# Optimization experiments

Measured on AMD Instinct MI355X. Metric: run time of the kernel, lower is better.

## Reference

```python
import jax, jax.numpy as jnp
import numpy as np
from jax import lax

B, S, T = 256, 128, 64
IN, MID, HID = 4, 128, 512
NH = 4  # attention heads


def setup_inputs() -> dict:
    key = jax.random.key(0)
    ks = iter(jax.random.split(key, 64))
    def p(*shape):
        return jax.random.normal(next(ks), shape, jnp.float32) * 0.05
    d = {}
    d["src"] = jax.random.normal(next(ks), (B, S, IN), jnp.float32)
    d["trg"] = jax.random.normal(next(ks), (B, T, IN), jnp.float32)
    # fc_in: IN -> MID//4 -> MID//2 -> MID
    d["fi_w1"] = p(MID // 4, IN); d["fi_b1"] = p(MID // 4)
    d["fi_w2"] = p(MID // 2, MID // 4); d["fi_b2"] = p(MID // 2)
    d["fi_w3"] = p(MID, MID // 2); d["fi_b3"] = p(MID)
    # encoder: 2-layer bidirectional LSTM (layer0 in=MID, layer1 in=2*HID)
    for name, ind in [("e0", MID), ("e1", 2 * HID)]:
        for sfx in ["f", "b"]:
            d[name + sfx + "_wih"] = p(4 * HID, ind)
            d[name + sfx + "_whh"] = p(4 * HID, HID)
            d[name + sfx + "_bih"] = p(4 * HID)
            d[name + sfx + "_bhh"] = p(4 * HID)
    d["attnfc_w"] = p(MID, 2 * HID); d["attnfc_b"] = p(MID)
    d["inproj_w"] = p(3 * MID, MID); d["inproj_b"] = p(3 * MID)
    d["outproj_w"] = p(MID, MID); d["outproj_b"] = p(MID)
    # decoder: 2-layer unidirectional LSTM (layer0 in=MID, layer1 in=HID)
    for name, ind in [("d0", MID), ("d1", HID)]:
        d[name + "_wih"] = p(4 * HID, ind)
        d[name + "_whh"] = p(4 * HID, HID)
        d[name + "_bih"] = p(4 * HID)
        d[name + "_bhh"] = p(4 * HID)
    # fc_out: HID -> MID//2 -> MID//4 -> IN
    d["fo_w1"] = p(MID // 2, HID); d["fo_b1"] = p(MID // 2)
    d["fo_w2"] = p(MID // 4, MID // 2); d["fo_b2"] = p(MID // 4)
    d["fo_w3"] = p(IN, MID // 4); d["fo_b3"] = p(IN)
    return d


def _gelu(x):
    return jax.nn.gelu(x, approximate=False)  # torch default GELU is exact


def _mlp3(x, w1, b1, w2, b2, w3, b3):
    h = _gelu(x @ w1.T + b1)
    h = _gelu(h @ w2.T + b2)
    return h @ w3.T + b3


def _lstm(x, h0, c0, wih, whh, bih, bhh, reverse=False):
    """PyTorch-semantics LSTM layer. x: (B,T,in) -> (hs (B,T,H), h_T, c_T)."""
    xg = jnp.einsum('bti,gi->btg', x, wih) + (bih + bhh)  # fold input GEMM over time
    def step(carry, xt):
        h, c = carry
        g = xt + h @ whh.T
        i, f, gg, o = jnp.split(g, 4, axis=-1)  # torch gate order: i,f,g,o
        c = jax.nn.sigmoid(f) * c + jax.nn.sigmoid(i) * jnp.tanh(gg)
        h = jax.nn.sigmoid(o) * jnp.tanh(c)
        return (h, c), h
    (h, c), hs = lax.scan(step, (h0, c0), jnp.swapaxes(xg, 0, 1), reverse=reverse)
    return jnp.swapaxes(hs, 0, 1), h, c


def _mha(q_in, kv, inproj_w, inproj_b, outproj_w, outproj_b):
    E = q_in.shape[-1]
    dh = E // NH
    wq, wk, wv = jnp.split(inproj_w, 3, axis=0)
    bq, bk, bv = jnp.split(inproj_b, 3)
    q = q_in @ wq.T + bq
    k = kv @ wk.T + bk
    v = kv @ wv.T + bv
    hd = lambda x: x.reshape(x.shape[0], x.shape[1], NH, dh)
    scores = jnp.einsum('bqhd,bkhd->bhqk', hd(q), hd(k)) * (1.0 / float(np.sqrt(dh)))
    a = jax.nn.softmax(scores, axis=-1)
    o = jnp.einsum('bhqk,bkhd->bqhd', a, hd(v)).reshape(q.shape)
    return o @ outproj_w.T + outproj_b


def reference(src, trg,
              fi_w1, fi_b1, fi_w2, fi_b2, fi_w3, fi_b3,
              e0f_wih, e0f_whh, e0f_bih, e0f_bhh, e0b_wih, e0b_whh, e0b_bih, e0b_bhh,
              e1f_wih, e1f_whh, e1f_bih, e1f_bhh, e1b_wih, e1b_whh, e1b_bih, e1b_bhh,
              attnfc_w, attnfc_b, inproj_w, inproj_b, outproj_w, outproj_b,
              d0_wih, d0_whh, d0_bih, d0_bhh, d1_wih, d1_whh, d1_bih, d1_bhh,
              fo_w1, fo_b1, fo_w2, fo_b2, fo_w3, fo_b3):
    bsz = src.shape[0]
    z = jnp.zeros((bsz, HID), src.dtype)
    enc_embed = _mlp3(src, fi_w1, fi_b1, fi_w2, fi_b2, fi_w3, fi_b3)
    # encoder layer 0 (bidirectional)
    l0f, hf0, cf0 = _lstm(enc_embed, z, z, e0f_wih, e0f_whh, e0f_bih, e0f_bhh)
    l0b, hb0, cb0 = _lstm(enc_embed, z, z, e0b_wih, e0b_whh, e0b_bih, e0b_bhh, reverse=True)
    x1 = jnp.concatenate([l0f, l0b], axis=-1)
    # encoder layer 1 (bidirectional)
    l1f, hf1, cf1 = _lstm(x1, z, z, e1f_wih, e1f_whh, e1f_bih, e1f_bhh)
    l1b, hb1, cb1 = _lstm(x1, z, z, e1b_wih, e1b_whh, e1b_bih, e1b_bhh, reverse=True)
    enc_out = jnp.concatenate([l1f, l1b], axis=-1)  # (B,S,2H)
    # h.view(L,2,B,H).sum(dim=1): sum forward+backward final states per layer
    h_l0, c_l0 = hf0 + hb0, cf0 + cb0
    h_l1, c_l1 = hf1 + hb1, cf1 + cb1
    proj_enc = jnp.tanh(enc_out @ attnfc_w.T + attnfc_b)  # (B,S,MID)
    # teacher_forcing_ratio = 1.0 -> decoder inputs are exactly trg[:, 0:T]
    inp = _mlp3(trg, fi_w1, fi_b1, fi_w2, fi_b2, fi_w3, fi_b3)  # (B,T,MID)
    attn_out = _mha(inp, proj_enc, inproj_w, inproj_b, outproj_w, outproj_b)
    dec_input = inp + attn_out
    d0, _, _ = _lstm(dec_input, h_l0, c_l0, d0_wih, d0_whh, d0_bih, d0_bhh)
    d1, _, _ = _lstm(d0, h_l1, c_l1, d1_wih, d1_whh, d1_bih, d1_bhh)
    delta = _mlp3(d1, fo_w1, fo_b1, fo_w2, fo_b2, fo_w3, fo_b3)
    return trg + delta  # pred_t = trg[:, t-1] + delta_t
```

## Files before the change

### kernel.cpp

```cpp
#include <hip/hip_runtime.h>
#include <cstdint>
#include <cstddef>
#include <cstdio>

typedef __bf16 bf16;
typedef __bf16 bf16x8 __attribute__((ext_vector_type(8)));
typedef __bf16 bf16x4 __attribute__((ext_vector_type(4)));
typedef float f32x4 __attribute__((ext_vector_type(4)));

#define DEVFN __device__ __forceinline__

DEVFN float geluf(float x) { return 0.5f * x * (1.0f + erff(x * 0.70710678118654752f)); }
DEVFN float sigmoidf(float x) { return 1.0f / (1.0f + expf(-x)); }

template <int WGM, int WGN, int ACT, bool RES>
__launch_bounds__(WGM * WGN * 64)
__global__ void gemm_bt(const bf16* __restrict__ A, const bf16* __restrict__ W,
                        const float* __restrict__ bias, const bf16* __restrict__ Rsd,
                        bf16* __restrict__ C, int M, int N, int K) {
  constexpr int BM = WGM * 64, BN = WGN * 64, T = WGM * WGN * 64;
  constexpr int NA = BM * 4 / T, NB = BN * 4 / T;
  __shared__ __align__(16) char ldsA[BM * 64];
  __shared__ __align__(16) char ldsB[BN * 64];
  const int tid = threadIdx.x;
  const int lane = tid & 63, wave = tid >> 6;
  const int wm = wave % WGM, wn = wave / WGM;
  const int l16 = lane & 15, quad = lane >> 4;
  const int bm0 = blockIdx.x * BM, bn0 = blockIdx.y * BN;

  f32x4 acc[4][4] = {};
  for (int k0 = 0; k0 < K; k0 += 32) {
    bf16x8 ta[NA], tb[NB];
#pragma unroll
    for (int i = 0; i < NA; ++i) {
      int lin = i * T + tid;
      int row = lin >> 2, seg = lin & 3;
      ta[i] = *(const bf16x8*)(A + (size_t)(bm0 + row) * K + k0 + seg * 8);
    }
#pragma unroll
    for (int i = 0; i < NB; ++i) {
      int lin = i * T + tid;
      int row = lin >> 2, seg = lin & 3;
      tb[i] = *(const bf16x8*)(W + (size_t)(bn0 + row) * K + k0 + seg * 8);
    }
#pragma unroll
    for (int i = 0; i < NA; ++i) *(bf16x8*)(ldsA + (i * T + tid) * 16) = ta[i];
#pragma unroll
    for (int i = 0; i < NB; ++i) *(bf16x8*)(ldsB + (i * T + tid) * 16) = tb[i];
    __syncthreads();
    bf16x8 af[4], bfrag[4];
#pragma unroll
    for (int mi = 0; mi < 4; ++mi)
      af[mi] = *(const bf16x8*)(ldsA + (wm * 64 + mi * 16 + l16) * 64 + quad * 16);
#pragma unroll
    for (int ni = 0; ni < 4; ++ni)
      bfrag[ni] = *(const bf16x8*)(ldsB + (wn * 64 + ni * 16 + l16) * 64 + quad * 16);
#pragma unroll
    for (int mi = 0; mi < 4; ++mi)
#pragma unroll
      for (int ni = 0; ni < 4; ++ni)
        acc[mi][ni] = __builtin_amdgcn_mfma_f32_16x16x32_bf16(af[mi], bfrag[ni], acc[mi][ni], 0, 0, 0);
    __syncthreads();
  }
#pragma unroll
  for (int mi = 0; mi < 4; ++mi) {
#pragma unroll
    for (int ni = 0; ni < 4; ++ni) {
      int col = bn0 + wn * 64 + ni * 16 + l16;
      float bv = bias[col];
#pragma unroll
      for (int r = 0; r < 4; ++r) {
        int row = bm0 + wm * 64 + mi * 16 + quad * 4 + r;
        float x = acc[mi][ni][r] + bv;
        if (ACT == 1) x = tanhf(x);
        if (ACT == 2) x = geluf(x);
        size_t idx = (size_t)row * N + col;
        if (RES) x += (float)Rsd[idx];
        C[idx] = (bf16)x;
      }
    }
  }
}

__launch_bounds__(128)
__global__ void gemm_hc_fcout(const bf16* __restrict__ HC, const bf16* __restrict__ W,
                              const float* __restrict__ bias, bf16* __restrict__ C,
                              int M, int N, int K) {
  constexpr int WGM = 2, WGN = 1;
  constexpr int BM = WGM * 64, BN = WGN * 64, T = WGM * WGN * 64;
  constexpr int NA = BM * 4 / T, NB = BN * 4 / T;
  __shared__ __align__(16) char ldsA[BM * 64];
  __shared__ __align__(16) char ldsB[BN * 64];
  const int tid = threadIdx.x;
  const int lane = tid & 63, wave = tid >> 6;
  const int wm = wave % WGM, wn = wave / WGM;
  const int l16 = lane & 15, quad = lane >> 4;
  const int bm0 = blockIdx.x * BM, bn0 = blockIdx.y * BN;

  f32x4 acc[4][4] = {};
  for (int k0 = 0; k0 < K; k0 += 32) {
    bf16x8 ta[NA], tb[NB];
#pragma unroll
    for (int i = 0; i < NA; ++i) {
      int lin = i * T + tid;
      int row = bm0 + (lin >> 2), seg = lin & 3;
      int t = row >> 8, b = row & 255;
      ta[i] = *(const bf16x8*)(HC + (size_t)t * 131072 + (size_t)((k0 >> 3) + seg) * 2048 + b * 8);
    }
#pragma unroll
    for (int i = 0; i < NB; ++i) {
      int lin = i * T + tid;
      int row = lin >> 2, seg = lin & 3;
      tb[i] = *(const bf16x8*)(W + (size_t)(bn0 + row) * K + k0 + seg * 8);
    }
#pragma unroll
    for (int i = 0; i < NA; ++i) *(bf16x8*)(ldsA + (i * T + tid) * 16) = ta[i];
#pragma unroll
    for (int i = 0; i < NB; ++i) *(bf16x8*)(ldsB + (i * T + tid) * 16) = tb[i];
    __syncthreads();
    bf16x8 af[4], bfrag[4];
#pragma unroll
    for (int mi = 0; mi < 4; ++mi)
      af[mi] = *(const bf16x8*)(ldsA + (wm * 64 + mi * 16 + l16) * 64 + quad * 16);
#pragma unroll
    for (int ni = 0; ni < 4; ++ni)
      bfrag[ni] = *(const bf16x8*)(ldsB + (wn * 64 + ni * 16 + l16) * 64 + quad * 16);
#pragma unroll
    for (int mi = 0; mi < 4; ++mi)
#pragma unroll
      for (int ni = 0; ni < 4; ++ni)
        acc[mi][ni] = __builtin_amdgcn_mfma_f32_16x16x32_bf16(af[mi], bfrag[ni], acc[mi][ni], 0, 0, 0);
    __syncthreads();
  }
#pragma unroll
  for (int mi = 0; mi < 4; ++mi) {
#pragma unroll
    for (int ni = 0; ni < 4; ++ni) {
      int col = bn0 + wn * 64 + ni * 16 + l16;
      float bv = bias[col];
#pragma unroll
      for (int r = 0; r < 4; ++r) {
        int row = bm0 + wm * 64 + mi * 16 + quad * 4 + r;
        float x = geluf(acc[mi][ni][r] + bv);
        C[(size_t)row * N + col] = (bf16)x;
      }
    }
  }
}

struct RDir {
  const bf16* whh_r;
  const bf16* xg;
  bf16* seq;
  bf16* hcomm;
  long long os_t, os_b;
  int ocol0, rev;
  const bf16* h0;
  float* cbuf;
  bf16* hfin;
};

__launch_bounds__(512, 1)
__global__ void lstm_rec(RDir da, RDir db, int t0, int tc, int Tfull, int* __restrict__ cnts) {
  const int blk = blockIdx.x;
  const RDir d = (blk >= 64) ? db : da;
  const int slice = blk & 63;
  const int colBase = slice * 32, unitBase = slice * 8;
  const int tid = threadIdx.x;
  const int w = tid >> 6, lane = tid & 63;
  const int l16 = lane & 15, quad = lane >> 4;

  __shared__ __align__(16) bf16 whh_lds[32 * 512];
  __shared__ __align__(16) bf16 hstg[256 * 8];

  for (int e = tid * 8; e < 32 * 512; e += 512 * 8) {
    int c = e >> 9, k0 = e & 511;
    bf16x8 v = *(const bf16x8*)(d.whh_r + (size_t)(colBase + c) * 512 + k0);
    *(bf16x8*)(whh_lds + ((k0 >> 3) << 8) + (c << 3)) = v;
  }
  float cst[2][2];
#pragma unroll
  for (int m = 0; m < 2; ++m)
#pragma unroll
    for (int i = 0; i < 2; ++i) {
      int b = (w * 2 + i) * 16 + l16;
      cst[m][i] = d.cbuf[(size_t)b * 512 + unitBase + m * 4 + quad];
    }
  __syncthreads();

  int* cnt = cnts + (blk & 64);
  const int b0 = (w * 2) * 16 + l16;
  const int b1 = b0 + 16;

  for (int s = 0; s < tc; ++s) {
    const int sg = t0 + s;
    const int t = d.rev ? (Tfull - 1 - sg) : sg;
    const int lt = d.rev ? (tc - 1 - s) : s;

    bf16x4 gxr[2][2];
#pragma unroll
    for (int m = 0; m < 2; ++m)
#pragma unroll
      for (int i = 0; i < 2; ++i) {
        int b = b0 + i * 16;
        gxr[m][i] = *(const bf16x4*)(d.xg + ((size_t)lt * 256 + b) * 2048 + colBase + m * 16 + quad * 4);
      }
    bf16x8 hr[16][2];
    if (sg == 0) {
      const bf16* hp0 = d.h0 + (size_t)b0 * 512 + quad * 8;
      const bf16* hp1 = d.h0 + (size_t)b1 * 512 + quad * 8;
#pragma unroll
      for (int kk = 0; kk < 16; ++kk) {
        hr[kk][0] = *(const bf16x8*)(hp0 + kk * 32);
        hr[kk][1] = *(const bf16x8*)(hp1 + kk * 32);
      }
    } else {
      const bf16* hc = d.hcomm + (size_t)(s - 1) * 131072;
#pragma unroll
      for (int kk = 0; kk < 16; ++kk) {
        int u8 = kk * 4 + quad;
        hr[kk][0] = *(const bf16x8*)(hc + u8 * 2048 + (size_t)b0 * 8);
        hr[kk][1] = *(const bf16x8*)(hc + u8 * 2048 + (size_t)b1 * 8);
      }
    }
    __builtin_amdgcn_sched_barrier(0);

    f32x4 acc[2][2] = {};
#pragma unroll
    for (int kk = 0; kk < 16; ++kk) {
      bf16x8 a0 = *(const bf16x8*)(whh_lds + kk * 1024 + quad * 256 + l16 * 8);
      bf16x8 a1 = *(const bf16x8*)(whh_lds + kk * 1024 + quad * 256 + 128 + l16 * 8);
      acc[0][0] = __builtin_amdgcn_mfma_f32_16x16x32_bf16(a0, hr[kk][0], acc[0][0], 0, 0, 0);
      acc[1][0] = __builtin_amdgcn_mfma_f32_16x16x32_bf16(a1, hr[kk][0], acc[1][0], 0, 0, 0);
      acc[0][1] = __builtin_amdgcn_mfma_f32_16x16x32_bf16(a0, hr[kk][1], acc[0][1], 0, 0, 0);
      acc[1][1] = __builtin_amdgcn_mfma_f32_16x16x32_bf16(a1, hr[kk][1], acc[1][1], 0, 0, 0);
    }
#pragma unroll
    for (int m = 0; m < 2; ++m)
#pragma unroll
      for (int i = 0; i < 2; ++i) {
        float gi = acc[m][i][0] + (float)gxr[m][i][0];
        float gf = acc[m][i][1] + (float)gxr[m][i][1];
        float gg = acc[m][i][2] + (float)gxr[m][i][2];
        float go = acc[m][i][3] + (float)gxr[m][i][3];
        float cn = sigmoidf(gf) * cst[m][i] + sigmoidf(gi) * tanhf(gg);
        float hv = sigmoidf(go) * tanhf(cn);
        cst[m][i] = cn;
        int b = (w * 2 + i) * 16 + l16;
        hstg[b * 8 + m * 4 + quad] = (bf16)hv;
      }
    __syncthreads();
    {
      unsigned long long v = *(const unsigned long long*)(hstg + tid * 4);
      __hip_atomic_store((unsigned long long*)(d.hcomm + (size_t)s * 131072 + slice * 2048 + tid * 4),
                         v, __ATOMIC_RELAXED, __HIP_MEMORY_SCOPE_AGENT);
    }
    __syncthreads();
    if (s < tc - 1 && tid == 0)
      __hip_atomic_fetch_add(cnt, 1, __ATOMIC_RELAXED, __HIP_MEMORY_SCOPE_AGENT);
    if (tid < 256) {
      const unsigned long long* p = (const unsigned long long*)(hstg + tid * 8);
      unsigned long long v0 = p[0], v1 = p[1];
      unsigned long long* q = (unsigned long long*)(d.seq + (size_t)t * d.os_t +
                                                    (size_t)tid * d.os_b + d.ocol0 + unitBase);
      q[0] = v0; q[1] = v1;
      if (sg == Tfull - 1 && d.hfin) {
        unsigned long long* r2 = (unsigned long long*)(d.hfin + (size_t)tid * 512 + unitBase);
        r2[0] = v0; r2[1] = v1;
      }
    }
    if (s < tc - 1) {
      if (w == 0) {
        int target = 64 * (s + 1), guard = 0;
        while (__hip_atomic_load(cnt, __ATOMIC_RELAXED, __HIP_MEMORY_SCOPE_AGENT) < target) {
          __builtin_amdgcn_s_sleep(2);
          if (++guard > (1 << 22)) break;
        }
      }
      __syncthreads();
    }
  }
#pragma unroll
  for (int m = 0; m < 2; ++m)
#pragma unroll
    for (int i = 0; i < 2; ++i) {
      int b = (w * 2 + i) * 16 + l16;
      d.cbuf[(size_t)b * 512 + unitBase + m * 4 + quad] = cst[m][i];
    }
}

__launch_bounds__(512, 1)
__global__ void lstm_dec_fused(
    const bf16* __restrict__ whh0, const bf16* __restrict__ xg0,
    bf16* __restrict__ hc0, const bf16* __restrict__ h0d0, float* __restrict__ c0buf,
    const bf16* __restrict__ whh1, const bf16* __restrict__ wih1, const float* __restrict__ bias1,
    bf16* __restrict__ hc1, const bf16* __restrict__ h0d1,
    float* __restrict__ c1buf, int* __restrict__ cnts) {
  const int blk = blockIdx.x;
  const int tid = threadIdx.x;
  const int w = tid >> 6, lane = tid & 63;
  const int l16 = lane & 15, quad = lane >> 4;
  constexpr int TC = 64;

  __shared__ __align__(16) bf16 wldsA[32 * 512];
  __shared__ __align__(16) bf16 wldsB[32 * 512];
  __shared__ __align__(16) bf16 hstg[256 * 8];

  int* cnt0 = cnts;
  int* cnt1 = cnts + 64;
  const int b0 = (w * 2) * 16 + l16;
  const int b1 = b0 + 16;

  if (blk < 64) {
    const int slice = blk;
    const int colBase = slice * 32;
    for (int e = tid * 8; e < 32 * 512; e += 512 * 8) {
      int c = e >> 9, k0 = e & 511;
      bf16x8 v = *(const bf16x8*)(whh0 + (size_t)(colBase + c) * 512 + k0);
      *(bf16x8*)(wldsA + ((k0 >> 3) << 8) + (c << 3)) = v;
    }
    float cst[2][2];
#pragma unroll
    for (int m = 0; m < 2; ++m)
#pragma unroll
      for (int i = 0; i < 2; ++i) {
        int b = (w * 2 + i) * 16 + l16;
        cst[m][i] = c0buf[(size_t)b * 512 + slice * 8 + m * 4 + quad];
      }
    __syncthreads();

    for (int s = 0; s < TC; ++s) {
      bf16x4 gxr[2][2];
#pragma unroll
      for (int m = 0; m < 2; ++m)
#pragma unroll
        for (int i = 0; i < 2; ++i) {
          int b = b0 + i * 16;
          gxr[m][i] = *(const bf16x4*)(xg0 + ((size_t)s * 256 + b) * 2048 + colBase + m * 16 + quad * 4);
        }
      bf16x8 hr[16][2];
      if (s == 0) {
        const bf16* hp0 = h0d0 + (size_t)b0 * 512 + quad * 8;
        const bf16* hp1 = h0d0 + (size_t)b1 * 512 + quad * 8;
#pragma unroll
        for (int kk = 0; kk < 16; ++kk) {
          hr[kk][0] = *(const bf16x8*)(hp0 + kk * 32);
          hr[kk][1] = *(const bf16x8*)(hp1 + kk * 32);
        }
      } else {
        const bf16* hc = hc0 + (size_t)(s - 1) * 131072;
#pragma unroll
        for (int kk = 0; kk < 16; ++kk) {
          int u8 = kk * 4 + quad;
          hr[kk][0] = *(const bf16x8*)(hc + u8 * 2048 + (size_t)b0 * 8);
          hr[kk][1] = *(const bf16x8*)(hc + u8 * 2048 + (size_t)b1 * 8);
        }
      }
      __builtin_amdgcn_sched_barrier(0);
      f32x4 acc[2][2] = {};
#pragma unroll
      for (int kk = 0; kk < 16; ++kk) {
        bf16x8 a0 = *(const bf16x8*)(wldsA + kk * 1024 + quad * 256 + l16 * 8);
        bf16x8 a1 = *(const bf16x8*)(wldsA + kk * 1024 + quad * 256 + 128 + l16 * 8);
        acc[0][0] = __builtin_amdgcn_mfma_f32_16x16x32_bf16(a0, hr[kk][0], acc[0][0], 0, 0, 0);
        acc[1][0] = __builtin_amdgcn_mfma_f32_16x16x32_bf16(a1, hr[kk][0], acc[1][0], 0, 0, 0);
        acc[0][1] = __builtin_amdgcn_mfma_f32_16x16x32_bf16(a0, hr[kk][1], acc[0][1], 0, 0, 0);
        acc[1][1] = __builtin_amdgcn_mfma_f32_16x16x32_bf16(a1, hr[kk][1], acc[1][1], 0, 0, 0);
      }
#pragma unroll
      for (int m = 0; m < 2; ++m)
#pragma unroll
        for (int i = 0; i < 2; ++i) {
          float gi = acc[m][i][0] + (float)gxr[m][i][0];
          float gf = acc[m][i][1] + (float)gxr[m][i][1];
          float gg = acc[m][i][2] + (float)gxr[m][i][2];
          float go = acc[m][i][3] + (float)gxr[m][i][3];
          float cn = sigmoidf(gf) * cst[m][i] + sigmoidf(gi) * tanhf(gg);
          float hv = sigmoidf(go) * tanhf(cn);
          cst[m][i] = cn;
          int b = (w * 2 + i) * 16 + l16;
          hstg[b * 8 + m * 4 + quad] = (bf16)hv;
        }
      __syncthreads();
      {
        unsigned long long v = *(const unsigned long long*)(hstg + tid * 4);
        __hip_atomic_store((unsigned long long*)(hc0 + (size_t)s * 131072 + slice * 2048 + tid * 4),
                           v, __ATOMIC_RELAXED, __HIP_MEMORY_SCOPE_AGENT);
      }
      __syncthreads();
      if (tid == 0)
        __hip_atomic_fetch_add(cnt0, 1, __ATOMIC_RELAXED, __HIP_MEMORY_SCOPE_AGENT);
      if (s < TC - 1) {
        if (w == 0) {
          int target = 64 * (s + 1), guard = 0;
          while (__hip_atomic_load(cnt0, __ATOMIC_RELAXED, __HIP_MEMORY_SCOPE_AGENT) < target) {
            __builtin_amdgcn_s_sleep(2);
            if (++guard > (1 << 22)) break;
          }
        }
        __syncthreads();
      }
    }
#pragma unroll
    for (int m = 0; m < 2; ++m)
#pragma unroll
      for (int i = 0; i < 2; ++i) {
        int b = (w * 2 + i) * 16 + l16;
        c0buf[(size_t)b * 512 + slice * 8 + m * 4 + quad] = cst[m][i];
      }
  } else {
    const int slice = blk - 64;
    const int colBase = slice * 32;
    for (int e = tid * 8; e < 32 * 512; e += 512 * 8) {
      int c = e >> 9, k0 = e & 511;
      bf16x8 v = *(const bf16x8*)(whh1 + (size_t)(colBase + c) * 512 + k0);
      *(bf16x8*)(wldsA + ((k0 >> 3) << 8) + (c << 3)) = v;
      bf16x8 u = *(const bf16x8*)(wih1 + (size_t)(colBase + c) * 512 + k0);
      *(bf16x8*)(wldsB + ((k0 >> 3) << 8) + (c << 3)) = u;
    }
    float gbv[2][4];
#pragma unroll
    for (int m = 0; m < 2; ++m)
#pragma unroll
      for (int r = 0; r < 4; ++r) gbv[m][r] = bias1[colBase + m * 16 + quad * 4 + r];
    float cst[2][2];
#pragma unroll
    for (int m = 0; m < 2; ++m)
#pragma unroll
      for (int i = 0; i < 2; ++i) {
        int b = (w * 2 + i) * 16 + l16;
        cst[m][i] = c1buf[(size_t)b * 512 + slice * 8 + m * 4 + quad];
      }
    __syncthreads();
    if (w == 0) {
      int guard = 0;
      while (__hip_atomic_load(cnt0, __ATOMIC_RELAXED, __HIP_MEMORY_SCOPE_AGENT) < 64) {
        __builtin_amdgcn_s_sleep(2);
        if (++guard > (1 << 22)) break;
      }
    }
    __syncthreads();

    for (int s = 0; s < TC; ++s) {
      f32x4 acc[2][2] = {};
      {
        const bf16* xc = hc0 + (size_t)s * 131072;
        bf16x8 xr[16][2];
#pragma unroll
        for (int kk = 0; kk < 16; ++kk) {
          int u8 = kk * 4 + quad;
          xr[kk][0] = *(const bf16x8*)(xc + u8 * 2048 + (size_t)b0 * 8);
          xr[kk][1] = *(const bf16x8*)(xc + u8 * 2048 + (size_t)b1 * 8);
        }
        __builtin_amdgcn_sched_barrier(0);
#pragma unroll
        for (int kk = 0; kk < 16; ++kk) {
          bf16x8 aw0 = *(const bf16x8*)(wldsB + kk * 1024 + quad * 256 + l16 * 8);
          bf16x8 aw1 = *(const bf16x8*)(wldsB + kk * 1024 + quad * 256 + 128 + l16 * 8);
          acc[0][0] = __builtin_amdgcn_mfma_f32_16x16x32_bf16(aw0, xr[kk][0], acc[0][0], 0, 0, 0);
          acc[1][0] = __builtin_amdgcn_mfma_f32_16x16x32_bf16(aw1, xr[kk][0], acc[1][0], 0, 0, 0);
          acc[0][1] = __builtin_amdgcn_mfma_f32_16x16x32_bf16(aw0, xr[kk][1], acc[0][1], 0, 0, 0);
          acc[1][1] = __builtin_amdgcn_mfma_f32_16x16x32_bf16(aw1, xr[kk][1], acc[1][1], 0, 0, 0);
        }
      }
      {
        bf16x8 hr[16][2];
        if (s == 0) {
          const bf16* hp0 = h0d1 + (size_t)b0 * 512 + quad * 8;
          const bf16* hp1 = h0d1 + (size_t)b1 * 512 + quad * 8;
#pragma unroll
          for (int kk = 0; kk < 16; ++kk) {
            hr[kk][0] = *(const bf16x8*)(hp0 + kk * 32);
            hr[kk][1] = *(const bf16x8*)(hp1 + kk * 32);
          }
        } else {
          const bf16* hc = hc1 + (size_t)(s - 1) * 131072;
#pragma unroll
          for (int kk = 0; kk < 16; ++kk) {
            int u8 = kk * 4 + quad;
            hr[kk][0] = *(const bf16x8*)(hc + u8 * 2048 + (size_t)b0 * 8);
            hr[kk][1] = *(const bf16x8*)(hc + u8 * 2048 + (size_t)b1 * 8);
          }
        }
        __builtin_amdgcn_sched_barrier(0);
#pragma unroll
        for (int kk = 0; kk < 16; ++kk) {
          bf16x8 a0 = *(const bf16x8*)(wldsA + kk * 1024 + quad * 256 + l16 * 8);
          bf16x8 a1 = *(const bf16x8*)(wldsA + kk * 1024 + quad * 256 + 128 + l16 * 8);
          acc[0][0] = __builtin_amdgcn_mfma_f32_16x16x32_bf16(a0, hr[kk][0], acc[0][0], 0, 0, 0);
          acc[1][0] = __builtin_amdgcn_mfma_f32_16x16x32_bf16(a1, hr[kk][0], acc[1][0], 0, 0, 0);
          acc[0][1] = __builtin_amdgcn_mfma_f32_16x16x32_bf16(a0, hr[kk][1], acc[0][1], 0, 0, 0);
          acc[1][1] = __builtin_amdgcn_mfma_f32_16x16x32_bf16(a1, hr[kk][1], acc[1][1], 0, 0, 0);
        }
      }
#pragma unroll
      for (int m = 0; m < 2; ++m)
#pragma unroll
        for (int i = 0; i < 2; ++i) {
          float gi = acc[m][i][0] + gbv[m][0];
          float gf = acc[m][i][1] + gbv[m][1];
          float gg = acc[m][i][2] + gbv[m][2];
          float go = acc[m][i][3] + gbv[m][3];
          float cn = sigmoidf(gf) * cst[m][i] + sigmoidf(gi) * tanhf(gg);
          float hv = sigmoidf(go) * tanhf(cn);
          cst[m][i] = cn;
          int b = (w * 2 + i) * 16 + l16;
          hstg[b * 8 + m * 4 + quad] = (bf16)hv;
        }
      __syncthreads();
      {
        unsigned long long v = *(const unsigned long long*)(hstg + tid * 4);
        __hip_atomic_store((unsigned long long*)(hc1 + (size_t)s * 131072 + slice * 2048 + tid * 4),
                           v, __ATOMIC_RELAXED, __HIP_MEMORY_SCOPE_AGENT);
      }
      __syncthreads();
      if (s < TC - 1) {
        if (tid == 0)
          __hip_atomic_fetch_add(cnt1, 1, __ATOMIC_RELAXED, __HIP_MEMORY_SCOPE_AGENT);
        if (w == 0) {
          int t1 = 64 * (s + 1), t0n = 64 * (s + 2), guard = 0;
          while (true) {
            int v1 = __hip_atomic_load(cnt1, __ATOMIC_RELAXED, __HIP_MEMORY_SCOPE_AGENT);
            int v0 = __hip_atomic_load(cnt0, __ATOMIC_RELAXED, __HIP_MEMORY_SCOPE_AGENT);
            if (v1 >= t1 && v0 >= t0n) break;
            __builtin_amdgcn_s_sleep(2);
            if (++guard > (1 << 22)) break;
          }
        }
        __syncthreads();
      }
    }
#pragma unroll
    for (int m = 0; m < 2; ++m)
#pragma unroll
      for (int i = 0; i < 2; ++i) {
        int b = (w * 2 + i) * 16 + l16;
        c1buf[(size_t)b * 512 + slice * 8 + m * 4 + quad] = cst[m][i];
      }
  }
}

__launch_bounds__(256)
__global__ void fc_in_mlp(const float* __restrict__ x, bf16* __restrict__ y, int rows, int tmod,
                          const float* __restrict__ w1, const float* __restrict__ b1,
                          const float* __restrict__ w2, const float* __restrict__ b2,
                          const float* __restrict__ w3, const float* __restrict__ b3) {
  __shared__ float sm[10592];
  const int tid = threadIdx.x;
  for (int i = tid; i < 10592; i += 256) {
    float v;
    if (i < 128) v = w1[i];
    else if (i < 160) v = b1[i - 128];
    else if (i < 2208) v = w2[i - 160];
    else if (i < 2272) v = b2[i - 2208];
    else if (i < 10464) v = w3[i - 2272];
    else v = b3[i - 10464];
    sm[i] = v;
  }
  __syncthreads();
  int row = blockIdx.x * 256 + tid;
  if (row >= rows) return;
  int orow = tmod ? ((row % tmod) * 256 + row / tmod) : row;
  float xin[4];
#pragma unroll
  for (int k = 0; k < 4; ++k) xin[k] = x[(size_t)row * 4 + k];
  float h1[32];
#pragma unroll
  for (int j = 0; j < 32; ++j) {
    float a = sm[128 + j];
#pragma unroll
    for (int k = 0; k < 4; ++k) a += sm[j * 4 + k] * xin[k];
    h1[j] = geluf(a);
  }
  float h2[64];
#pragma unroll
  for (int j = 0; j < 64; ++j) {
    float a = sm[2208 + j];
#pragma unroll
    for (int k = 0; k < 32; ++k) a += sm[160 + j * 32 + k] * h1[k];
    h2[j] = geluf(a);
  }
  for (int c = 0; c < 8; ++c) {
    float accv[16];
#pragma unroll
    for (int j = 0; j < 16; ++j) accv[j] = sm[10464 + c * 16 + j];
#pragma unroll
    for (int j = 0; j < 16; ++j) {
#pragma unroll
      for (int k = 0; k < 64; ++k) accv[j] += sm[2272 + (c * 16 + j) * 64 + k] * h2[k];
    }
#pragma unroll
    for (int j = 0; j < 16; ++j) y[(size_t)orow * 128 + c * 16 + j] = (bf16)accv[j];
  }
}

__launch_bounds__(256)
__global__ void fc_out_tail(const bf16* __restrict__ h1in, const float* __restrict__ trg,
                            float* __restrict__ out, int rows,
                            const float* __restrict__ w2, const float* __restrict__ b2,
                            const float* __restrict__ w3, const float* __restrict__ b3) {
  __shared__ float sm[2212];
  const int tid = threadIdx.x;
  for (int i = tid; i < 2212; i += 256) {
    float v;
    if (i < 2048) v = w2[i];
    else if (i < 2080) v = b2[i - 2048];
    else if (i < 2208) v = w3[i - 2080];
    else v = b3[i - 2208];
    sm[i] = v;
  }
  __syncthreads();
  int row = blockIdx.x * 256 + tid;
  if (row >= rows) return;
  int b = row >> 6, t = row & 63;
  const bf16* h1p = h1in + ((size_t)t * 256 + b) * 64;
  float h1[64];
#pragma unroll
  for (int k = 0; k < 64; ++k) h1[k] = (float)h1p[k];
  float h2[32];
#pragma unroll
  for (int j = 0; j < 32; ++j) {
    float a = sm[2048 + j];
#pragma unroll
    for (int k = 0; k < 64; ++k) a += sm[j * 64 + k] * h1[k];
    h2[j] = geluf(a);
  }
#pragma unroll
  for (int dd = 0; dd < 4; ++dd) {
    float a = sm[2208 + dd];
#pragma unroll
    for (int k = 0; k < 32; ++k) a += sm[2080 + dd * 32 + k] * h2[k];
    out[(size_t)row * 4 + dd] = trg[(size_t)row * 4 + dd] + a;
  }
}

__launch_bounds__(128)
__global__ void attention_kernel(const bf16* __restrict__ Q, const bf16* __restrict__ K,
                                 const bf16* __restrict__ V, bf16* __restrict__ O) {
  __shared__ bf16 qs[64 * 32];
  __shared__ float ks[128 * 33];
  __shared__ bf16 vs[128 * 32];
  __shared__ float sc[64 * 132];
  const int b = blockIdx.x, h = blockIdx.y, tid = threadIdx.x;
  for (int i = tid; i < 64 * 32; i += 128) {
    int t = i >> 5, dd = i & 31;
    qs[i] = Q[((size_t)t * 256 + b) * 128 + h * 32 + dd];
  }
  for (int i = tid; i < 128 * 32; i += 128) {
    int s = i >> 5, dd = i & 31;
    size_t ridx = ((size_t)s * 256 + b) * 128 + h * 32 + dd;
    ks[s * 33 + dd] = (float)K[ridx];
    vs[i] = V[ridx];
  }
  __syncthreads();
  const float scale = 0.17677669529663687f;
  for (int i = tid; i < 64 * 128; i += 128) {
    int t = i >> 7, s = i & 127;
    float a = 0.f;
#pragma unroll
    for (int dd = 0; dd < 32; ++dd) a += (float)qs[t * 32 + dd] * ks[s * 33 + dd];
    sc[t * 132 + s] = a * scale;
  }
  __syncthreads();
  if (tid < 64) {
    float m = -1e30f;
    for (int s = 0; s < 128; ++s) m = fmaxf(m, sc[tid * 132 + s]);
    float sum = 0.f;
    for (int s = 0; s < 128; ++s) { float e = expf(sc[tid * 132 + s] - m); sc[tid * 132 + s] = e; sum += e; }
    float r = 1.0f / sum;
    for (int s = 0; s < 128; ++s) sc[tid * 132 + s] *= r;
  }
  __syncthreads();
  for (int i = tid; i < 64 * 32; i += 128) {
    int t = i >> 5, dd = i & 31;
    float a = 0.f;
    for (int s = 0; s < 128; ++s) a += sc[t * 132 + s] * (float)vs[s * 32 + dd];
    O[((size_t)t * 256 + b) * 128 + h * 32 + dd] = (bf16)a;
  }
}

__global__ void reorder_gate_rows(const float* __restrict__ in, bf16* __restrict__ out, int K) {
  int i = blockIdx.x * 256 + threadIdx.x;
  if (i >= 2048 * K) return;
  int r = i / K, k = i - r * K;
  int nr = 4 * (r & 511) + (r >> 9);
  out[(size_t)nr * K + k] = (bf16)in[i];
}

__global__ void combine_bias(const float* __restrict__ a, const float* __restrict__ b,
                             float* __restrict__ out) {
  int i = blockIdx.x * 256 + threadIdx.x;
  if (i >= 2048) return;
  out[4 * (i & 511) + (i >> 9)] = a[i] + b[i];
}

__global__ void f2b(const float* __restrict__ in, bf16* __restrict__ out, int n) {
  int i = blockIdx.x * 256 + threadIdx.x;
  if (i < n) out[i] = (bf16)in[i];
}

__global__ void zero_u32(uint32_t* __restrict__ p, int n) {
  int i = blockIdx.x * 256 + threadIdx.x;
  if (i < n) p[i] = 0u;
}

__global__ void dec_state_init(const bf16* __restrict__ hf, const bf16* __restrict__ hb,
                               const float* __restrict__ cf, const float* __restrict__ cb,
                               bf16* __restrict__ hout, float* __restrict__ cout) {
  int i = blockIdx.x * 256 + threadIdx.x;
  if (i >= 256 * 512) return;
  hout[i] = (bf16)((float)hf[i] + (float)hb[i]);
  cout[i] = cf[i] + cb[i];
}

extern "C" void kernel_launch(void* const* d_in, const int* in_sizes, int n_in,
                              void* d_out, int out_size, void* d_ws, size_t ws_size,
                              hipStream_t stream) {
  (void)in_sizes; (void)n_in; (void)out_size;
  const float* src = (const float*)d_in[0];
  const float* trg = (const float*)d_in[1];
  const float* fi_w1 = (const float*)d_in[2];
  const float* fi_b1 = (const float*)d_in[3];
  const float* fi_w2 = (const float*)d_in[4];
  const float* fi_b2 = (const float*)d_in[5];
  const float* fi_w3 = (const float*)d_in[6];
  const float* fi_b3 = (const float*)d_in[7];
  const float* wih_in[6] = {(const float*)d_in[8],  (const float*)d_in[12], (const float*)d_in[16],
                            (const float*)d_in[20], (const float*)d_in[30], (const float*)d_in[34]};
  const float* whh_in[6] = {(const float*)d_in[9],  (const float*)d_in[13], (const float*)d_in[17],
                            (const float*)d_in[21], (const float*)d_in[31], (const float*)d_in[35]};
  const float* bih_in[6] = {(const float*)d_in[10], (const float*)d_in[14], (const float*)d_in[18],
                            (const float*)d_in[22], (const float*)d_in[32], (const float*)d_in[36]};
  const float* bhh_in[6] = {(const float*)d_in[11], (const float*)d_in[15], (const float*)d_in[19],
                            (const float*)d_in[23], (const float*)d_in[33], (const float*)d_in[37]};
  const int kin[6] = {128, 128, 1024, 1024, 128, 512};
  const float* attnfc_w = (const float*)d_in[24];
  const float* attnfc_b = (const float*)d_in[25];
  const float* inproj_w = (const float*)d_in[26];
  const float* inproj_b = (const float*)d_in[27];
  const float* outproj_w = (const float*)d_in[28];
  const float* outproj_b = (const float*)d_in[29];
  const float* fo_w1 = (const float*)d_in[38];
  const float* fo_b1 = (const float*)d_in[39];
  const float* fo_w2 = (const float*)d_in[40];
  const float* fo_b2 = (const float*)d_in[41];
  const float* fo_w3 = (const float*)d_in[42];
  const float* fo_b3 = (const float*)d_in[43];
  float* out = (float*)d_out;

  char* base = (char*)d_ws;
  size_t o = 0;
  auto take = [&](size_t bytes) -> char* {
    char* p = base + o;
    o = (o + bytes + 255) & ~(size_t)255;
    return p;
  };
  bf16* wr_wih[6]; for (int i = 0; i < 6; ++i) wr_wih[i] = (bf16*)take((size_t)2048 * kin[i] * 2);
  bf16* wr_whh[6]; for (int i = 0; i < 6; ++i) wr_whh[i] = (bf16*)take((size_t)2048 * 512 * 2);
  float* bias_l[6]; for (int i = 0; i < 6; ++i) bias_l[i] = (float*)take(2048 * 4);
  bf16* attnfc_wb = (bf16*)take((size_t)128 * 1024 * 2);
  bf16* inproj_wb = (bf16*)take((size_t)384 * 128 * 2);
  bf16* outproj_wb = (bf16*)take((size_t)128 * 128 * 2);
  bf16* fo_w1b = (bf16*)take((size_t)64 * 512 * 2);
  bf16* h0_0 = (bf16*)take((size_t)6 * 256 * 512 * 2);
  bf16* hf_0 = (bf16*)take((size_t)6 * 256 * 512 * 2);
  float* c_0 = (float*)take((size_t)6 * 256 * 512 * 4);
  int* flags = (int*)take(2048 * 4);
  bf16* hcE = (bf16*)take((size_t)16 << 20);
  bf16* h0_[6]; bf16* hf_[6]; float* c_[6];
  for (int i = 0; i < 6; ++i) {
    h0_[i] = h0_0 + (size_t)i * 256 * 512;
    hf_[i] = hf_0 + (size_t)i * 256 * 512;
    c_[i] = c_0 + (size_t)i * 256 * 512;
  }
  char* RA = take((size_t)64 << 20);
  char* RB = take((size_t)64 << 20);
  char* XG = take((size_t)64 << 20);
  bf16* embed = (bf16*)take((size_t)32768 * 128 * 2);
  size_t required = o;
  if (required > ws_size) {
    fprintf(stderr, "[kernel_launch] ws_size=%zu < required=%zu — aborting launch\n",
            ws_size, required);
    return;
  }

  bf16* x1       = (bf16*)RA;
  bf16* proj_enc = (bf16*)RA;
  bf16* inp      = (bf16*)(RA + ((size_t)8 << 20));
  bf16* qb       = (bf16*)(RA + ((size_t)12 << 20));
  bf16* kb       = (bf16*)(RA + ((size_t)16 << 20));
  bf16* vb       = (bf16*)(RA + ((size_t)24 << 20));
  bf16* attnb    = (bf16*)(RA + ((size_t)32 << 20));
  bf16* dec_in   = (bf16*)(RA + ((size_t)36 << 20));
  bf16* fc1out   = (bf16*)(RA + ((size_t)40 << 20));
  bf16* enc_out  = (bf16*)RB;
  bf16* hc0      = (bf16*)RB;
  bf16* hc1      = (bf16*)(RB + ((size_t)20 << 20));
  bf16* xgA      = (bf16*)XG;
  bf16* xgB      = (bf16*)(XG + ((size_t)32 << 20));
  bf16* xg_dec   = (bf16*)XG;

  for (int i = 0; i < 6; ++i) {
    reorder_gate_rows<<<dim3((2048 * kin[i] + 255) / 256), 256, 0, stream>>>(wih_in[i], wr_wih[i], kin[i]);
    reorder_gate_rows<<<dim3(4096), 256, 0, stream>>>(whh_in[i], wr_whh[i], 512);
    combine_bias<<<dim3(8), 256, 0, stream>>>(bih_in[i], bhh_in[i], bias_l[i]);
  }
  f2b<<<dim3(512), 256, 0, stream>>>(attnfc_w, attnfc_wb, 128 * 1024);
  f2b<<<dim3(192), 256, 0, stream>>>(inproj_w, inproj_wb, 384 * 128);
  f2b<<<dim3(64), 256, 0, stream>>>(outproj_w, outproj_wb, 128 * 128);
  f2b<<<dim3(128), 256, 0, stream>>>(fo_w1, fo_w1b, 64 * 512);
  zero_u32<<<dim3(1024), 256, 0, stream>>>((uint32_t*)h0_0, 4 * 256 * 512 / 2);
  zero_u32<<<dim3(2048), 256, 0, stream>>>((uint32_t*)c_0, 4 * 256 * 512);
  zero_u32<<<dim3(8), 256, 0, stream>>>((uint32_t*)flags, 2048);

  fc_in_mlp<<<dim3(128), 256, 0, stream>>>(src, embed, 32768, 128, fi_w1, fi_b1, fi_w2, fi_b2, fi_w3, fi_b3);

  for (int layer = 0; layer < 2; ++layer) {
    const bf16* lin = layer ? x1 : embed;
    bf16* lout = layer ? enc_out : x1;
    int K2 = kin[layer * 2];
    int wf = layer * 2, wb = layer * 2 + 1;
    for (int c = 0; c < 4; ++c) {
      int t0 = c * 32;
      gemm_bt<2, 2, 0, false><<<dim3(64, 16), 256, 0, stream>>>(
          lin + (size_t)t0 * 256 * K2, wr_wih[wf], bias_l[wf], nullptr, xgA, 8192, 2048, K2);
      gemm_bt<2, 2, 0, false><<<dim3(64, 16), 256, 0, stream>>>(
          lin + (size_t)(128 - t0 - 32) * 256 * K2, wr_wih[wb], bias_l[wb], nullptr, xgB, 8192, 2048, K2);
      RDir f{wr_whh[wf], xgA, lout, hcE, 262144, 1024, 0, 0, h0_[wf], c_[wf], hf_[wf]};
      RDir bk{wr_whh[wb], xgB, lout, hcE + (size_t)32 * 131072, 262144, 1024, 512, 1, h0_[wb], c_[wb], hf_[wb]};
      lstm_rec<<<dim3(128), 512, 0, stream>>>(f, bk, t0, 32, 128, flags + layer * 512 + c * 128);
    }
  }

  gemm_bt<2, 2, 1, false><<<dim3(256, 1), 256, 0, stream>>>(enc_out, attnfc_wb, attnfc_b, nullptr, proj_enc, 32768, 128, 1024);

  fc_in_mlp<<<dim3(64), 256, 0, stream>>>(trg, inp, 16384, 64, fi_w1, fi_b1, fi_w2, fi_b2, fi_w3, fi_b3);

  gemm_bt<2, 2, 0, false><<<dim3(128, 1), 256, 0, stream>>>(inp, inproj_wb, inproj_b, nullptr, qb, 16384, 128, 128);
  gemm_bt<2, 2, 0, false><<<dim3(256, 1), 256, 0, stream>>>(proj_enc, inproj_wb + (size_t)128 * 128, inproj_b + 128, nullptr, kb, 32768, 128, 128);
  gemm_bt<2, 2, 0, false><<<dim3(256, 1), 256, 0, stream>>>(proj_enc, inproj_wb + (size_t)256 * 128, inproj_b + 256, nullptr, vb, 32768, 128, 128);
  attention_kernel<<<dim3(256, 4), 128, 0, stream>>>(qb, kb, vb, attnb);
  gemm_bt<2, 2, 0, true><<<dim3(128, 1), 256, 0, stream>>>(attnb, outproj_wb, outproj_b, inp, dec_in, 16384, 128, 128);

  dec_state_init<<<dim3(512), 256, 0, stream>>>(hf_[0], hf_[1], c_[0], c_[1], h0_[4], c_[4]);
  dec_state_init<<<dim3(512), 256, 0, stream>>>(hf_[2], hf_[3], c_[2], c_[3], h0_[5], c_[5]);

  gemm_bt<2, 2, 0, false><<<dim3(128, 16), 256, 0, stream>>>(dec_in, wr_wih[4], bias_l[4], nullptr, xg_dec, 16384, 2048, 128);
  lstm_dec_fused<<<dim3(128), 512, 0, stream>>>(
      wr_whh[4], xg_dec, hc0, h0_[4], c_[4],
      wr_whh[5], wr_wih[5], bias_l[5], hc1, h0_[5], c_[5],
      flags + 1024);

  gemm_hc_fcout<<<dim3(128, 1), 128, 0, stream>>>(hc1, fo_w1b, fo_b1, fc1out, 16384, 64, 512);
  fc_out_tail<<<dim3(64), 256, 0, stream>>>(fc1out, trg, out, 16384, fo_w2, fo_b2, fo_w3, fo_b3);
}
```

Before: 3.639 ms.

## Store encoder LSTM outputs in communication layout and read directly in GEMMs

The encoder LSTM no longer writes a separate row-major sequence output. Its per-step hidden communication buffer is now laid out per timestep and doubles as the layer output. A new GEMM variant reads this slice-major layout directly as the A operand for the layer-1 input projection and the attention fc. This removes the duplicate sequence store from the latency-critical recurrent loop and drops a workspace buffer. The cost is strided A-operand gathers with 16-byte segments in the GEMMs.

```diff
diff --git a/kernel.cpp b/kernel.cpp
--- a/kernel.cpp
+++ b/kernel.cpp
@@ -82,6 +82,74 @@
   }
 }
 
+template <int WGM, int WGN, int ACT>
+__launch_bounds__(WGM * WGN * 64)
+__global__ void gemm_hcA(const bf16* __restrict__ HC, int tbase, const bf16* __restrict__ W,
+                         const float* __restrict__ bias, bf16* __restrict__ C,
+                         int M, int N, int K) {
+  constexpr int BM = WGM * 64, BN = WGN * 64, T = WGM * WGN * 64;
+  constexpr int NA = BM * 4 / T, NB = BN * 4 / T;
+  __shared__ __align__(16) char ldsA[BM * 64];
+  __shared__ __align__(16) char ldsB[BN * 64];
+  const int tid = threadIdx.x;
+  const int lane = tid & 63, wave = tid >> 6;
+  const int wm = wave % WGM, wn = wave / WGM;
+  const int l16 = lane & 15, quad = lane >> 4;
+  const int bm0 = blockIdx.x * BM, bn0 = blockIdx.y * BN;
+
+  f32x4 acc[4][4] = {};
+  for (int k0 = 0; k0 < K; k0 += 32) {
+    bf16x8 ta[NA], tb[NB];
+#pragma unroll
+    for (int i = 0; i < NA; ++i) {
+      int lin = i * T + tid;
+      int row = bm0 + (lin >> 2), seg = lin & 3;
+      int t = tbase + (row >> 8), b = row & 255;
+      ta[i] = *(const bf16x8*)(HC + (size_t)t * 262144 + (size_t)((k0 >> 3) + seg) * 2048 + b * 8);
+    }
+#pragma unroll
+    for (int i = 0; i < NB; ++i) {
+      int lin = i * T + tid;
+      int row = lin >> 2, seg = lin & 3;
+      tb[i] = *(const bf16x8*)(W + (size_t)(bn0 + row) * K + k0 + seg * 8);
+    }
+#pragma unroll
+    for (int i = 0; i < NA; ++i) *(bf16x8*)(ldsA + (i * T + tid) * 16) = ta[i];
+#pragma unroll
+    for (int i = 0; i < NB; ++i) *(bf16x8*)(ldsB + (i * T + tid) * 16) = tb[i];
+    __syncthreads();
+    bf16x8 af[4], bfrag[4];
+#pragma unroll
+    for (int mi = 0; mi < 4; ++mi)
+      af[mi] = *(const bf16x8*)(ldsA + (wm * 64 + mi * 16 + l16) * 64 + quad * 16);
+#pragma unroll
+    for (int ni = 0; ni < 4; ++ni)
+      bfrag[ni] = *(const bf16x8*)(ldsB + (wn * 64 + ni * 16 + l16) * 64 + quad * 16);
+#pragma unroll
+    for (int mi = 0; mi < 4; ++mi)
+#pragma unroll
+      for (int ni = 0; ni < 4; ++ni)
+        acc[mi][ni] = __builtin_amdgcn_mfma_f32_16x16x32_bf16(af[mi], bfrag[ni], acc[mi][ni], 0, 0, 0);
+    __syncthreads();
+  }
+#pragma unroll
+  for (int mi = 0; mi < 4; ++mi) {
+#pragma unroll
+    for (int ni = 0; ni < 4; ++ni) {
+      int col = bn0 + wn * 64 + ni * 16 + l16;
+      float bv = bias[col];
+#pragma unroll
+      for (int r = 0; r < 4; ++r) {
+        int row = bm0 + wm * 64 + mi * 16 + quad * 4 + r;
+        float x = acc[mi][ni][r] + bv;
+        if (ACT == 1) x = tanhf(x);
+        if (ACT == 2) x = geluf(x);
+        C[(size_t)row * N + col] = (bf16)x;
+      }
+    }
+  }
+}
+
 __launch_bounds__(128)
 __global__ void gemm_hc_fcout(const bf16* __restrict__ HC, const bf16* __restrict__ W,
                               const float* __restrict__ bias, bf16* __restrict__ C,
@@ -151,10 +219,8 @@
 struct RDir {
   const bf16* whh_r;
   const bf16* xg;
-  bf16* seq;
-  bf16* hcomm;
-  long long os_t, os_b;
-  int ocol0, rev;
+  bf16* hc;
+  int slcOff, rev;
   const bf16* h0;
   float* cbuf;
   bf16* hfin;
@@ -215,7 +281,8 @@
         hr[kk][1] = *(const bf16x8*)(hp1 + kk * 32);
       }
     } else {
-      const bf16* hc = d.hcomm + (size_t)(s - 1) * 131072;
+      const int tp = d.rev ? (t + 1) : (t - 1);
+      const bf16* hc = d.hc + (size_t)tp * 262144 + (size_t)d.slcOff * 2048;
 #pragma unroll
       for (int kk = 0; kk < 16; ++kk) {
         int u8 = kk * 4 + quad;
@@ -252,22 +319,17 @@
     __syncthreads();
     {
       unsigned long long v = *(const unsigned long long*)(hstg + tid * 4);
-      __hip_atomic_store((unsigned long long*)(d.hcomm + (size_t)s * 131072 + slice * 2048 + tid * 4),
+      __hip_atomic_store((unsigned long long*)(d.hc + (size_t)t * 262144 +
+                                               (size_t)(d.slcOff + slice) * 2048 + tid * 4),
                          v, __ATOMIC_RELAXED, __HIP_MEMORY_SCOPE_AGENT);
     }
     __syncthreads();
     if (s < tc - 1 && tid == 0)
       __hip_atomic_fetch_add(cnt, 1, __ATOMIC_RELAXED, __HIP_MEMORY_SCOPE_AGENT);
-    if (tid < 256) {
+    if (sg == Tfull - 1 && d.hfin && tid < 256) {
       const unsigned long long* p = (const unsigned long long*)(hstg + tid * 8);
-      unsigned long long v0 = p[0], v1 = p[1];
-      unsigned long long* q = (unsigned long long*)(d.seq + (size_t)t * d.os_t +
-                                                    (size_t)tid * d.os_b + d.ocol0 + unitBase);
-      q[0] = v0; q[1] = v1;
-      if (sg == Tfull - 1 && d.hfin) {
-        unsigned long long* r2 = (unsigned long long*)(d.hfin + (size_t)tid * 512 + unitBase);
-        r2[0] = v0; r2[1] = v1;
-      }
+      unsigned long long* r2 = (unsigned long long*)(d.hfin + (size_t)tid * 512 + unitBase);
+      r2[0] = p[0]; r2[1] = p[1];
     }
     if (s < tc - 1) {
       if (w == 0) {
@@ -766,7 +828,6 @@
   bf16* hf_0 = (bf16*)take((size_t)6 * 256 * 512 * 2);
   float* c_0 = (float*)take((size_t)6 * 256 * 512 * 4);
   int* flags = (int*)take(2048 * 4);
-  bf16* hcE = (bf16*)take((size_t)16 << 20);
   bf16* h0_[6]; bf16* hf_[6]; float* c_[6];
   for (int i = 0; i < 6; ++i) {
     h0_[i] = h0_0 + (size_t)i * 256 * 512;
@@ -784,7 +845,7 @@
     return;
   }
 
-  bf16* x1       = (bf16*)RA;
+  bf16* x1_hc    = (bf16*)RA;
   bf16* proj_enc = (bf16*)RA;
   bf16* inp      = (bf16*)(RA + ((size_t)8 << 20));
   bf16* qb       = (bf16*)(RA + ((size_t)12 << 20));
@@ -793,7 +854,7 @@
   bf16* attnb    = (bf16*)(RA + ((size_t)32 << 20));
   bf16* dec_in   = (bf16*)(RA + ((size_t)36 << 20));
   bf16* fc1out   = (bf16*)(RA + ((size_t)40 << 20));
-  bf16* enc_out  = (bf16*)RB;
+  bf16* enc_hc   = (bf16*)RB;
   bf16* hc0      = (bf16*)RB;
   bf16* hc1      = (bf16*)(RB + ((size_t)20 << 20));
   bf16* xgA      = (bf16*)XG;
@@ -815,24 +876,29 @@
 
   fc_in_mlp<<<dim3(128), 256, 0, stream>>>(src, embed, 32768, 128, fi_w1, fi_b1, fi_w2, fi_b2, fi_w3, fi_b3);
 
-  for (int layer = 0; layer < 2; ++layer) {
-    const bf16* lin = layer ? x1 : embed;
-    bf16* lout = layer ? enc_out : x1;
-    int K2 = kin[layer * 2];
-    int wf = layer * 2, wb = layer * 2 + 1;
-    for (int c = 0; c < 4; ++c) {
-      int t0 = c * 32;
-      gemm_bt<2, 2, 0, false><<<dim3(64, 16), 256, 0, stream>>>(
-          lin + (size_t)t0 * 256 * K2, wr_wih[wf], bias_l[wf], nullptr, xgA, 8192, 2048, K2);
-      gemm_bt<2, 2, 0, false><<<dim3(64, 16), 256, 0, stream>>>(
-          lin + (size_t)(128 - t0 - 32) * 256 * K2, wr_wih[wb], bias_l[wb], nullptr, xgB, 8192, 2048, K2);
-      RDir f{wr_whh[wf], xgA, lout, hcE, 262144, 1024, 0, 0, h0_[wf], c_[wf], hf_[wf]};
-      RDir bk{wr_whh[wb], xgB, lout, hcE + (size_t)32 * 131072, 262144, 1024, 512, 1, h0_[wb], c_[wb], hf_[wb]};
-      lstm_rec<<<dim3(128), 512, 0, stream>>>(f, bk, t0, 32, 128, flags + layer * 512 + c * 128);
-    }
-  }
-
-  gemm_bt<2, 2, 1, false><<<dim3(256, 1), 256, 0, stream>>>(enc_out, attnfc_wb, attnfc_b, nullptr, proj_enc, 32768, 128, 1024);
+  for (int c = 0; c < 4; ++c) {
+    int t0 = c * 32;
+    gemm_bt<2, 2, 0, false><<<dim3(64, 16), 256, 0, stream>>>(
+        embed + (size_t)t0 * 256 * 128, wr_wih[0], bias_l[0], nullptr, xgA, 8192, 2048, 128);
+    gemm_bt<2, 2, 0, false><<<dim3(64, 16), 256, 0, stream>>>(
+        embed + (size_t)(128 - t0 - 32) * 256 * 128, wr_wih[1], bias_l[1], nullptr, xgB, 8192, 2048, 128);
+    RDir f{wr_whh[0], xgA, x1_hc, 0, 0, h0_[0], c_[0], hf_[0]};
+    RDir bk{wr_whh[1], xgB, x1_hc, 64, 1, h0_[1], c_[1], hf_[1]};
+    lstm_rec<<<dim3(128), 512, 0, stream>>>(f, bk, t0, 32, 128, flags + c * 128);
+  }
+  for (int c = 0; c < 4; ++c) {
+    int t0 = c * 32;
+    gemm_hcA<2, 2, 0><<<dim3(64, 16), 256, 0, stream>>>(
+        x1_hc, t0, wr_wih[2], bias_l[2], xgA, 8192, 2048, 1024);
+    gemm_hcA<2, 2, 0><<<dim3(64, 16), 256, 0, stream>>>(
+        x1_hc, 128 - t0 - 32, wr_wih[3], bias_l[3], xgB, 8192, 2048, 1024);
+    RDir f{wr_whh[2], xgA, enc_hc, 0, 0, h0_[2], c_[2], hf_[2]};
+    RDir bk{wr_whh[3], xgB, enc_hc, 64, 1, h0_[3], c_[3], hf_[3]};
+    lstm_rec<<<dim3(128), 512, 0, stream>>>(f, bk, t0, 32, 128, flags + 512 + c * 128);
+  }
+
+  gemm_hcA<2, 2, 1><<<dim3(256, 1), 256, 0, stream>>>(
+      enc_hc, 0, attnfc_wb, attnfc_b, proj_enc, 32768, 128, 1024);
 
   fc_in_mlp<<<dim3(64), 256, 0, stream>>>(trg, inp, 16384, 64, fi_w1, fi_b1, fi_w2, fi_b2, fi_w3, fi_b3);
 
```

New measurement: 3.685 ms. About the same (+1.2%).
